# Optimization experiments

Hardware: AMD Instinct MI355X
Metric: run time of the kernel (lower is better)

The kernel has to match this reference:

```python
import jax, jax.numpy as jnp
import numpy as np

N, T, D, H = 256, 256, 1024, 1024


def setup_inputs() -> dict:
    key = jax.random.key(0)
    k1, k2, k3, k4, k5, k6 = jax.random.split(key, 6)
    encoded_subjects = jax.random.normal(k1, (N, T, D), dtype=jnp.float32)
    encoded_objects = jax.random.normal(k2, (N, T, D), dtype=jnp.float32)
    # pair_ffn: Linear(2D -> H), ReLU, Linear(H -> 1); torch Linear stores W as [out, in]
    lim1 = 1.0 / np.sqrt(2 * D)
    W1 = jax.random.uniform(k3, (H, 2 * D), dtype=jnp.float32, minval=-lim1, maxval=lim1)
    b1 = jax.random.uniform(k4, (H,), dtype=jnp.float32, minval=-lim1, maxval=lim1)
    lim2 = 1.0 / np.sqrt(H)
    W2 = jax.random.uniform(k5, (1, H), dtype=jnp.float32, minval=-lim2, maxval=lim2)
    b2 = jax.random.uniform(k6, (1,), dtype=jnp.float32, minval=-lim2, maxval=lim2)
    return {
        "encoded_subjects": encoded_subjects,
        "encoded_objects": encoded_objects,
        "W1": W1,
        "b1": b1,
        "W2": W2,
        "b2": b2,
    }


def reference(encoded_subjects, encoded_objects, W1, b1, W2, b2):
    # max-pool over token dim -> [N, D]
    sub = jnp.max(encoded_subjects, axis=1)
    obj = jnp.max(encoded_objects, axis=1)
    n = obj.shape[0]
    # cat([sub_i, obj_j]) @ W1.T == sub_i @ W1[:, :D].T + obj_j @ W1[:, D:].T
    d = sub.shape[-1]
    s_part = jnp.einsum("nd,hd->nh", sub, W1[:, :d])  # [N, H]
    o_part = jnp.einsum("nd,hd->nh", obj, W1[:, d:])  # [N, H]
    h = jax.nn.relu(s_part[:, None, :] + o_part[None, :, :] + b1)  # [N, N, H]
    scores = jnp.einsum("ijh,h->ij", h, W2[0]) + b2[0]  # [N, N]
    # diagonal entries stay zero (loop skips i == j)
    pair_matrix = jnp.where(jnp.eye(n, dtype=bool), 0.0, scores)
    return pair_matrix
```

## Files before the change

kernel.cpp:

```cpp
#include <hip/hip_runtime.h>
#include <math.h>

#define NN 256
#define TT 256
#define DD 1024
#define HH 1024

__global__ __launch_bounds__(256) void pool_kernel(const float* __restrict__ subs,
                                                   const float* __restrict__ objs,
                                                   float* __restrict__ pooled) {
    const int n = blockIdx.x;
    const int which = blockIdx.y;
    const float* src = (which == 0) ? subs : objs;
    const int d4 = threadIdx.x;
    const float4* base = reinterpret_cast<const float4*>(src + (size_t)n * TT * DD) + d4;

    float4 a0 = make_float4(-INFINITY, -INFINITY, -INFINITY, -INFINITY);
    float4 a1 = a0, a2 = a0, a3 = a0;
    for (int t = 0; t < TT; t += 4) {
        float4 v0 = base[(size_t)(t + 0) * (DD / 4)];
        float4 v1 = base[(size_t)(t + 1) * (DD / 4)];
        float4 v2 = base[(size_t)(t + 2) * (DD / 4)];
        float4 v3 = base[(size_t)(t + 3) * (DD / 4)];
        a0.x = fmaxf(a0.x, v0.x); a0.y = fmaxf(a0.y, v0.y); a0.z = fmaxf(a0.z, v0.z); a0.w = fmaxf(a0.w, v0.w);
        a1.x = fmaxf(a1.x, v1.x); a1.y = fmaxf(a1.y, v1.y); a1.z = fmaxf(a1.z, v1.z); a1.w = fmaxf(a1.w, v1.w);
        a2.x = fmaxf(a2.x, v2.x); a2.y = fmaxf(a2.y, v2.y); a2.z = fmaxf(a2.z, v2.z); a2.w = fmaxf(a2.w, v2.w);
        a3.x = fmaxf(a3.x, v3.x); a3.y = fmaxf(a3.y, v3.y); a3.z = fmaxf(a3.z, v3.z); a3.w = fmaxf(a3.w, v3.w);
    }
    float4 m;
    m.x = fmaxf(fmaxf(a0.x, a1.x), fmaxf(a2.x, a3.x));
    m.y = fmaxf(fmaxf(a0.y, a1.y), fmaxf(a2.y, a3.y));
    m.z = fmaxf(fmaxf(a0.z, a1.z), fmaxf(a2.z, a3.z));
    m.w = fmaxf(fmaxf(a0.w, a1.w), fmaxf(a2.w, a3.w));
    float4* dst = reinterpret_cast<float4*>(pooled + (size_t)(which * NN + n) * DD) + d4;
    *dst = m;
}

#define BM 32
#define BN 64
#define BK 32

__global__ __launch_bounds__(256) void gemm_kernel(const float* __restrict__ A,
                                                   const float* __restrict__ W1,
                                                   const float* __restrict__ b1,
                                                   float* __restrict__ out) {
    __shared__ float As[BK][BM];
    __shared__ float Bs[BK][BN];
    const int t = threadIdx.x;
    const int tx = t & 15, ty = t >> 4;
    const int m0 = blockIdx.y * BM;
    const int n0 = blockIdx.x * BN;
    const bool is_sub = (m0 < NN);
    const int koff = is_sub ? 0 : DD;

    const int a_m = t >> 3;
    const int a_k = (t & 7) * 4;
    const int b_n = t >> 3;
    const int b_k = (t & 7) * 4;

    const float* Aptr  = A  + (size_t)(m0 + a_m) * DD + a_k;
    const float* Bptr0 = W1 + (size_t)(n0 + b_n) * (2 * DD) + koff + b_k;
    const float* Bptr1 = W1 + (size_t)(n0 + 32 + b_n) * (2 * DD) + koff + b_k;

    float acc[2][4] = {{0.f, 0.f, 0.f, 0.f}, {0.f, 0.f, 0.f, 0.f}};

    float4 pa  = *(const float4*)(Aptr);
    float4 pb0 = *(const float4*)(Bptr0);
    float4 pb1 = *(const float4*)(Bptr1);
    As[a_k + 0][a_m] = pa.x;  As[a_k + 1][a_m] = pa.y;  As[a_k + 2][a_m] = pa.z;  As[a_k + 3][a_m] = pa.w;
    Bs[b_k + 0][b_n] = pb0.x; Bs[b_k + 1][b_n] = pb0.y; Bs[b_k + 2][b_n] = pb0.z; Bs[b_k + 3][b_n] = pb0.w;
    Bs[b_k + 0][b_n + 32] = pb1.x; Bs[b_k + 1][b_n + 32] = pb1.y;
    Bs[b_k + 2][b_n + 32] = pb1.z; Bs[b_k + 3][b_n + 32] = pb1.w;
    __syncthreads();

    const int NCHUNK = DD / BK;
    for (int c = 0; c < NCHUNK; ++c) {
        float4 na, nb0, nb1;
        if (c + 1 < NCHUNK) {
            const int off = (c + 1) * BK;
            na  = *(const float4*)(Aptr + off);
            nb0 = *(const float4*)(Bptr0 + off);
            nb1 = *(const float4*)(Bptr1 + off);
        }
#pragma unroll
        for (int k = 0; k < BK; ++k) {
            float2 a = *(const float2*)&As[k][ty * 2];
            float4 b = *(const float4*)&Bs[k][tx * 4];
            acc[0][0] += a.x * b.x; acc[0][1] += a.x * b.y;
            acc[0][2] += a.x * b.z; acc[0][3] += a.x * b.w;
            acc[1][0] += a.y * b.x; acc[1][1] += a.y * b.y;
            acc[1][2] += a.y * b.z; acc[1][3] += a.y * b.w;
        }
        __syncthreads();
        if (c + 1 < NCHUNK) {
            As[a_k + 0][a_m] = na.x;  As[a_k + 1][a_m] = na.y;
            As[a_k + 2][a_m] = na.z;  As[a_k + 3][a_m] = na.w;
            Bs[b_k + 0][b_n] = nb0.x; Bs[b_k + 1][b_n] = nb0.y;
            Bs[b_k + 2][b_n] = nb0.z; Bs[b_k + 3][b_n] = nb0.w;
            Bs[b_k + 0][b_n + 32] = nb1.x; Bs[b_k + 1][b_n + 32] = nb1.y;
            Bs[b_k + 2][b_n + 32] = nb1.z; Bs[b_k + 3][b_n + 32] = nb1.w;
            __syncthreads();
        }
    }

    float4 bias = make_float4(0.f, 0.f, 0.f, 0.f);
    if (is_sub) bias = *(const float4*)&b1[n0 + tx * 4];
#pragma unroll
    for (int mi = 0; mi < 2; ++mi) {
        const int mg = m0 + ty * 2 + mi;
        float4 r;
        r.x = acc[mi][0] + bias.x; r.y = acc[mi][1] + bias.y;
        r.z = acc[mi][2] + bias.z; r.w = acc[mi][3] + bias.w;
        *(float4*)&out[(size_t)mg * HH + n0 + tx * 4] = r;
    }
}

#define HC 128

__global__ __launch_bounds__(256) void pair_kernel(const float* __restrict__ sp_op,
                                                   const float* __restrict__ W2,
                                                   const float* __restrict__ b2,
                                                   float* __restrict__ out) {
    __shared__ float sT[16][HC + 4];
    __shared__ float oT[16][HC + 4];
    __shared__ float w2s[HH];
    const int t = threadIdx.x;
    const int tx = t & 15, ty = t >> 4;
    const int i0 = blockIdx.y * 16, j0 = blockIdx.x * 16;
    const float* sp = sp_op;
    const float* op = sp_op + (size_t)NN * HH;

    *(float4*)&w2s[t * 4] = *(const float4*)&W2[t * 4];

    const int s_row = t >> 5;
    const int s_h = (t & 31) * 4;

    float acc = 0.f;
    for (int c = 0; c < HH / HC; ++c) {
        __syncthreads();
#pragma unroll
        for (int r = 0; r < 2; ++r) {
            const int row = s_row + r * 8;
            *(float4*)&sT[row][s_h] = *(const float4*)&sp[(size_t)(i0 + row) * HH + c * HC + s_h];
            *(float4*)&oT[row][s_h] = *(const float4*)&op[(size_t)(j0 + row) * HH + c * HC + s_h];
        }
        __syncthreads();
#pragma unroll
        for (int h4 = 0; h4 < HC / 4; ++h4) {
            float4 s = *(const float4*)&sT[ty][h4 * 4];
            float4 o = *(const float4*)&oT[tx][h4 * 4];
            float4 w = *(const float4*)&w2s[c * HC + h4 * 4];
            acc += fmaxf(s.x + o.x, 0.f) * w.x;
            acc += fmaxf(s.y + o.y, 0.f) * w.y;
            acc += fmaxf(s.z + o.z, 0.f) * w.z;
            acc += fmaxf(s.w + o.w, 0.f) * w.w;
        }
    }
    const int i = i0 + ty, j = j0 + tx;
    const float score = acc + b2[0];
    out[i * NN + j] = (i == j) ? 0.f : score;
}

extern "C" void kernel_launch(void* const* d_in, const int* in_sizes, int n_in,
                              void* d_out, int out_size, void* d_ws, size_t ws_size,
                              hipStream_t stream) {
    const float* subs = (const float*)d_in[0];
    const float* objs = (const float*)d_in[1];
    const float* W1   = (const float*)d_in[2];
    const float* b1   = (const float*)d_in[3];
    const float* W2   = (const float*)d_in[4];
    const float* b2   = (const float*)d_in[5];
    float* out = (float*)d_out;

    float* pooled = (float*)d_ws;
    float* sp_op  = pooled + (size_t)2 * NN * DD;

    pool_kernel<<<dim3(NN, 2), 256, 0, stream>>>(subs, objs, pooled);
    gemm_kernel<<<dim3(HH / BN, (2 * NN) / BM), 256, 0, stream>>>(pooled, W1, b1, sp_op);
    pair_kernel<<<dim3(NN / 16, NN / 16), 256, 0, stream>>>(sp_op, W2, b2, out);
}
```

Baseline: 161.2 us.

## Split pooling over token chunks, retile GEMM with k-contiguous smem, prefetch pair tiles

Max-pooling now runs as 2048 blocks, each covering a quarter of the token range, and a small second kernel combines the four partial maxima. This is meant to fill the GPU while streaming the 512 MB input. The GEMM switches to a 64x32 tile with k-contiguous padded shared-memory rows written as float4, and each thread computes 4x2 outputs. The pair kernel register-prefetches the next H chunk and reads W2 straight from global memory instead of staging it in shared memory. In exchange there is an extra kernel launch and an extra partial buffer in workspace.

```diff
diff --git a/kernel.cpp b/kernel.cpp
--- a/kernel.cpp
+++ b/kernel.cpp
@@ -6,18 +6,20 @@
 #define DD 1024
 #define HH 1024
 
-__global__ __launch_bounds__(256) void pool_kernel(const float* __restrict__ subs,
-                                                   const float* __restrict__ objs,
-                                                   float* __restrict__ pooled) {
+__global__ __launch_bounds__(256) void pool_partial(const float* __restrict__ subs,
+                                                    const float* __restrict__ objs,
+                                                    float* __restrict__ partial) {
     const int n = blockIdx.x;
     const int which = blockIdx.y;
+    const int tc = blockIdx.z;
     const float* src = (which == 0) ? subs : objs;
     const int d4 = threadIdx.x;
-    const float4* base = reinterpret_cast<const float4*>(src + (size_t)n * TT * DD) + d4;
+    const float4* base = reinterpret_cast<const float4*>(src + (size_t)n * TT * DD) +
+                         (size_t)tc * 64 * (DD / 4) + d4;
 
     float4 a0 = make_float4(-INFINITY, -INFINITY, -INFINITY, -INFINITY);
     float4 a1 = a0, a2 = a0, a3 = a0;
-    for (int t = 0; t < TT; t += 4) {
+    for (int t = 0; t < 64; t += 4) {
         float4 v0 = base[(size_t)(t + 0) * (DD / 4)];
         float4 v1 = base[(size_t)(t + 1) * (DD / 4)];
         float4 v2 = base[(size_t)(t + 2) * (DD / 4)];
@@ -32,86 +34,113 @@
     m.y = fmaxf(fmaxf(a0.y, a1.y), fmaxf(a2.y, a3.y));
     m.z = fmaxf(fmaxf(a0.z, a1.z), fmaxf(a2.z, a3.z));
     m.w = fmaxf(fmaxf(a0.w, a1.w), fmaxf(a2.w, a3.w));
-    float4* dst = reinterpret_cast<float4*>(pooled + (size_t)(which * NN + n) * DD) + d4;
+    float4* dst = reinterpret_cast<float4*>(partial + ((size_t)(tc * 2 + which) * NN + n) * DD) + d4;
     *dst = m;
 }
 
-#define BM 32
-#define BN 64
+__global__ __launch_bounds__(256) void pool_reduce(const float* __restrict__ partial,
+                                                   float* __restrict__ pooled) {
+    const int row = blockIdx.x;
+    const int d4 = threadIdx.x;
+    const float4* p = reinterpret_cast<const float4*>(partial) + (size_t)row * (DD / 4) + d4;
+    const size_t stride = (size_t)2 * NN * (DD / 4);
+    float4 v0 = p[0];
+    float4 v1 = p[stride];
+    float4 v2 = p[2 * stride];
+    float4 v3 = p[3 * stride];
+    float4 m;
+    m.x = fmaxf(fmaxf(v0.x, v1.x), fmaxf(v2.x, v3.x));
+    m.y = fmaxf(fmaxf(v0.y, v1.y), fmaxf(v2.y, v3.y));
+    m.z = fmaxf(fmaxf(v0.z, v1.z), fmaxf(v2.z, v3.z));
+    m.w = fmaxf(fmaxf(v0.w, v1.w), fmaxf(v2.w, v3.w));
+    reinterpret_cast<float4*>(pooled)[(size_t)row * (DD / 4) + d4] = m;
+}
+
+#define BM 64
+#define BN 32
 #define BK 32
+#define LDP 36
 
 __global__ __launch_bounds__(256) void gemm_kernel(const float* __restrict__ A,
                                                    const float* __restrict__ W1,
                                                    const float* __restrict__ b1,
                                                    float* __restrict__ out) {
-    __shared__ float As[BK][BM];
-    __shared__ float Bs[BK][BN];
+    __shared__ float As[BM][LDP];
+    __shared__ float Bs[BN][LDP];
     const int t = threadIdx.x;
-    const int tx = t & 15, ty = t >> 4;
+    const int nx = t & 15;
+    const int tm = t >> 4;
     const int m0 = blockIdx.y * BM;
     const int n0 = blockIdx.x * BN;
     const bool is_sub = (m0 < NN);
     const int koff = is_sub ? 0 : DD;
 
-    const int a_m = t >> 3;
+    const int a_row = t >> 3;
     const int a_k = (t & 7) * 4;
-    const int b_n = t >> 3;
+    const int b_row = t >> 3;
     const int b_k = (t & 7) * 4;
 
-    const float* Aptr  = A  + (size_t)(m0 + a_m) * DD + a_k;
-    const float* Bptr0 = W1 + (size_t)(n0 + b_n) * (2 * DD) + koff + b_k;
-    const float* Bptr1 = W1 + (size_t)(n0 + 32 + b_n) * (2 * DD) + koff + b_k;
-
-    float acc[2][4] = {{0.f, 0.f, 0.f, 0.f}, {0.f, 0.f, 0.f, 0.f}};
-
-    float4 pa  = *(const float4*)(Aptr);
-    float4 pb0 = *(const float4*)(Bptr0);
-    float4 pb1 = *(const float4*)(Bptr1);
-    As[a_k + 0][a_m] = pa.x;  As[a_k + 1][a_m] = pa.y;  As[a_k + 2][a_m] = pa.z;  As[a_k + 3][a_m] = pa.w;
-    Bs[b_k + 0][b_n] = pb0.x; Bs[b_k + 1][b_n] = pb0.y; Bs[b_k + 2][b_n] = pb0.z; Bs[b_k + 3][b_n] = pb0.w;
-    Bs[b_k + 0][b_n + 32] = pb1.x; Bs[b_k + 1][b_n + 32] = pb1.y;
-    Bs[b_k + 2][b_n + 32] = pb1.z; Bs[b_k + 3][b_n + 32] = pb1.w;
+    const float* Aptr0 = A + (size_t)(m0 + a_row) * DD + a_k;
+    const float* Aptr1 = A + (size_t)(m0 + a_row + 32) * DD + a_k;
+    const float* Bptr = W1 + (size_t)(n0 + b_row) * (2 * DD) + koff + b_k;
+
+    float acc[4][2];
+#pragma unroll
+    for (int i = 0; i < 4; ++i) { acc[i][0] = 0.f; acc[i][1] = 0.f; }
+
+    float4 pa0 = *(const float4*)(Aptr0);
+    float4 pa1 = *(const float4*)(Aptr1);
+    float4 pb  = *(const float4*)(Bptr);
+    *(float4*)&As[a_row][a_k] = pa0;
+    *(float4*)&As[a_row + 32][a_k] = pa1;
+    *(float4*)&Bs[b_row][b_k] = pb;
     __syncthreads();
 
     const int NCHUNK = DD / BK;
     for (int c = 0; c < NCHUNK; ++c) {
-        float4 na, nb0, nb1;
+        float4 na0, na1, nb;
         if (c + 1 < NCHUNK) {
             const int off = (c + 1) * BK;
-            na  = *(const float4*)(Aptr + off);
-            nb0 = *(const float4*)(Bptr0 + off);
-            nb1 = *(const float4*)(Bptr1 + off);
-        }
-#pragma unroll
-        for (int k = 0; k < BK; ++k) {
-            float2 a = *(const float2*)&As[k][ty * 2];
-            float4 b = *(const float4*)&Bs[k][tx * 4];
-            acc[0][0] += a.x * b.x; acc[0][1] += a.x * b.y;
-            acc[0][2] += a.x * b.z; acc[0][3] += a.x * b.w;
-            acc[1][0] += a.y * b.x; acc[1][1] += a.y * b.y;
-            acc[1][2] += a.y * b.z; acc[1][3] += a.y * b.w;
+            na0 = *(const float4*)(Aptr0 + off);
+            na1 = *(const float4*)(Aptr1 + off);
+            nb  = *(const float4*)(Bptr + off);
+        }
+#pragma unroll
+        for (int kq = 0; kq < BK; kq += 4) {
+            float4 a[4], b[2];
+#pragma unroll
+            for (int i = 0; i < 4; ++i) a[i] = *(const float4*)&As[tm * 4 + i][kq];
+#pragma unroll
+            for (int j = 0; j < 2; ++j) b[j] = *(const float4*)&Bs[nx * 2 + j][kq];
+#pragma unroll
+            for (int i = 0; i < 4; ++i) {
+#pragma unroll
+                for (int j = 0; j < 2; ++j) {
+                    acc[i][j] += a[i].x * b[j].x;
+                    acc[i][j] += a[i].y * b[j].y;
+                    acc[i][j] += a[i].z * b[j].z;
+                    acc[i][j] += a[i].w * b[j].w;
+                }
+            }
         }
         __syncthreads();
         if (c + 1 < NCHUNK) {
-            As[a_k + 0][a_m] = na.x;  As[a_k + 1][a_m] = na.y;
-            As[a_k + 2][a_m] = na.z;  As[a_k + 3][a_m] = na.w;
-            Bs[b_k + 0][b_n] = nb0.x; Bs[b_k + 1][b_n] = nb0.y;
-            Bs[b_k + 2][b_n] = nb0.z; Bs[b_k + 3][b_n] = nb0.w;
-            Bs[b_k + 0][b_n + 32] = nb1.x; Bs[b_k + 1][b_n + 32] = nb1.y;
-            Bs[b_k + 2][b_n + 32] = nb1.z; Bs[b_k + 3][b_n + 32] = nb1.w;
+            *(float4*)&As[a_row][a_k] = na0;
+            *(float4*)&As[a_row + 32][a_k] = na1;
+            *(float4*)&Bs[b_row][b_k] = nb;
             __syncthreads();
         }
     }
 
-    float4 bias = make_float4(0.f, 0.f, 0.f, 0.f);
-    if (is_sub) bias = *(const float4*)&b1[n0 + tx * 4];
-#pragma unroll
-    for (int mi = 0; mi < 2; ++mi) {
-        const int mg = m0 + ty * 2 + mi;
-        float4 r;
-        r.x = acc[mi][0] + bias.x; r.y = acc[mi][1] + bias.y;
-        r.z = acc[mi][2] + bias.z; r.w = acc[mi][3] + bias.w;
-        *(float4*)&out[(size_t)mg * HH + n0 + tx * 4] = r;
+    float2 bias = make_float2(0.f, 0.f);
+    if (is_sub) bias = *(const float2*)&b1[n0 + nx * 2];
+#pragma unroll
+    for (int i = 0; i < 4; ++i) {
+        const int mg = m0 + tm * 4 + i;
+        float2 r;
+        r.x = acc[i][0] + bias.x;
+        r.y = acc[i][1] + bias.y;
+        *(float2*)&out[(size_t)mg * HH + n0 + nx * 2] = r;
     }
 }
 
@@ -123,38 +152,54 @@
                                                    float* __restrict__ out) {
     __shared__ float sT[16][HC + 4];
     __shared__ float oT[16][HC + 4];
-    __shared__ float w2s[HH];
     const int t = threadIdx.x;
     const int tx = t & 15, ty = t >> 4;
     const int i0 = blockIdx.y * 16, j0 = blockIdx.x * 16;
     const float* sp = sp_op;
     const float* op = sp_op + (size_t)NN * HH;
 
-    *(float4*)&w2s[t * 4] = *(const float4*)&W2[t * 4];
-
     const int s_row = t >> 5;
     const int s_h = (t & 31) * 4;
 
+    float4 rs[2], ro[2];
+#pragma unroll
+    for (int r = 0; r < 2; ++r) {
+        const int row = s_row + r * 8;
+        rs[r] = *(const float4*)&sp[(size_t)(i0 + row) * HH + s_h];
+        ro[r] = *(const float4*)&op[(size_t)(j0 + row) * HH + s_h];
+    }
+
     float acc = 0.f;
     for (int c = 0; c < HH / HC; ++c) {
-        __syncthreads();
 #pragma unroll
         for (int r = 0; r < 2; ++r) {
             const int row = s_row + r * 8;
-            *(float4*)&sT[row][s_h] = *(const float4*)&sp[(size_t)(i0 + row) * HH + c * HC + s_h];
-            *(float4*)&oT[row][s_h] = *(const float4*)&op[(size_t)(j0 + row) * HH + c * HC + s_h];
+            *(float4*)&sT[row][s_h] = rs[r];
+            *(float4*)&oT[row][s_h] = ro[r];
+        }
+        float4 ns[2], no[2];
+        if (c + 1 < HH / HC) {
+#pragma unroll
+            for (int r = 0; r < 2; ++r) {
+                const int row = s_row + r * 8;
+                ns[r] = *(const float4*)&sp[(size_t)(i0 + row) * HH + (c + 1) * HC + s_h];
+                no[r] = *(const float4*)&op[(size_t)(j0 + row) * HH + (c + 1) * HC + s_h];
+            }
         }
         __syncthreads();
 #pragma unroll
         for (int h4 = 0; h4 < HC / 4; ++h4) {
             float4 s = *(const float4*)&sT[ty][h4 * 4];
             float4 o = *(const float4*)&oT[tx][h4 * 4];
-            float4 w = *(const float4*)&w2s[c * HC + h4 * 4];
+            float4 w = *(const float4*)&W2[c * HC + h4 * 4];
             acc += fmaxf(s.x + o.x, 0.f) * w.x;
             acc += fmaxf(s.y + o.y, 0.f) * w.y;
             acc += fmaxf(s.z + o.z, 0.f) * w.z;
             acc += fmaxf(s.w + o.w, 0.f) * w.w;
         }
+        __syncthreads();
+#pragma unroll
+        for (int r = 0; r < 2; ++r) { rs[r] = ns[r]; ro[r] = no[r]; }
     }
     const int i = i0 + ty, j = j0 + tx;
     const float score = acc + b2[0];
@@ -172,10 +217,12 @@
     const float* b2   = (const float*)d_in[5];
     float* out = (float*)d_out;
 
-    float* pooled = (float*)d_ws;
-    float* sp_op  = pooled + (size_t)2 * NN * DD;
-
-    pool_kernel<<<dim3(NN, 2), 256, 0, stream>>>(subs, objs, pooled);
+    float* partial = (float*)d_ws;
+    float* pooled  = partial + (size_t)8 * NN * DD;
+    float* sp_op   = pooled + (size_t)2 * NN * DD;
+
+    pool_partial<<<dim3(NN, 2, 4), 256, 0, stream>>>(subs, objs, partial);
+    pool_reduce<<<dim3(2 * NN), 256, 0, stream>>>(partial, pooled);
     gemm_kernel<<<dim3(HH / BN, (2 * NN) / BM), 256, 0, stream>>>(pooled, W1, b1, sp_op);
     pair_kernel<<<dim3(NN / 16, NN / 16), 256, 0, stream>>>(sp_op, W2, b2, out);
 }
```

New measurement: 189.8 us. 1.18x slower.
